# Kernel optimization log

Measured on AMD Instinct MI355X. Metric: run time of the kernel, lower is better.

Reference implementation:

```python
import jax, jax.numpy as jnp
import numpy as np

B, L, IDIM = 1, 1024, 2048
H, DK, DV, K = 16, 128, 128, 4
KEY_DIM = H * DK          # 2048
VAL_DIM = H * DV          # 2048
CONV_DIM = 2 * KEY_DIM + VAL_DIM  # 6144
EPS = 1e-6


def setup_inputs() -> dict:
    key = jax.random.key(0)
    ks = jax.random.split(key, 8)
    s = 0.02
    x = jax.random.normal(ks[0], (B, L, IDIM), jnp.float32)
    Wqkv = jax.random.normal(ks[1], (IDIM, CONV_DIM), jnp.float32) * s
    Wz = jax.random.normal(ks[2], (IDIM, VAL_DIM), jnp.float32) * s
    Wb = jax.random.normal(ks[3], (IDIM, H), jnp.float32) * s
    Wa = jax.random.normal(ks[4], (IDIM, H), jnp.float32) * s
    conv_w = jax.random.normal(ks[5], (CONV_DIM, 1, K), jnp.float32) * 0.2  # depthwise [O,I/g=1,K]
    A_log = jnp.log(jax.random.uniform(ks[6], (H,), jnp.float32, 0.1, 16.0))
    dt_bias = jnp.ones((H,), jnp.float32)
    norm_w = jnp.ones((DV,), jnp.float32)
    Wout = jax.random.normal(ks[7], (VAL_DIM, IDIM), jnp.float32) * s
    return dict(x=x, Wqkv=Wqkv, Wz=Wz, Wb=Wb, Wa=Wa, conv_w=conv_w,
                A_log=A_log, dt_bias=dt_bias, norm_w=norm_w, Wout=Wout)


def _l2norm(t):
    return t * jax.lax.rsqrt(jnp.sum(t * t, axis=-1, keepdims=True) + EPS)


def reference(x, Wqkv, Wz, Wb, Wa, conv_w, A_log, dt_bias, norm_w, Wout):
    b, l, _ = x.shape
    # fused QKV projection + causal depthwise conv + SiLU
    qkv = jnp.einsum('bld,dc->blc', x, Wqkv)                 # [B,L,CONV_DIM]
    qkv = jnp.transpose(qkv, (0, 2, 1))                      # [B,C,L]
    qkv = jax.lax.conv_general_dilated(
        qkv, conv_w, window_strides=(1,), padding=[(K - 1, 0)],
        dimension_numbers=('NCL', 'OIL', 'NCL'), feature_group_count=CONV_DIM)
    qkv = jax.nn.silu(jnp.transpose(qkv, (0, 2, 1)))         # [B,L,C]
    q, k, v = jnp.split(qkv, [KEY_DIM, 2 * KEY_DIM], axis=-1)

    z = jnp.einsum('bld,dv->blv', x, Wz)                     # [B,L,VAL_DIM]
    beta = jax.nn.sigmoid(jnp.einsum('bld,dh->blh', x, Wb))  # [B,L,H]
    A = -jnp.exp(A_log)                                      # [H]
    dt = jax.nn.softplus(jnp.einsum('bld,dh->blh', x, Wa) + dt_bias)
    g = dt * A                                               # [B,L,H] (negative)

    q = _l2norm(q.reshape(b, l, H, DK))
    k = _l2norm(k.reshape(b, l, H, DK))
    v = v.reshape(b, l, H, DV)
    scale = DK ** -0.5

    # time-major for scan: [L,B,H,...]
    qs = jnp.transpose(q, (1, 0, 2, 3)) * scale
    ks_ = jnp.transpose(k, (1, 0, 2, 3))
    vs = jnp.transpose(v, (1, 0, 2, 3))
    bs = jnp.transpose(beta, (1, 0, 2))
    gs = jnp.transpose(g, (1, 0, 2))

    M0 = jnp.zeros((b, H, DK, DV), jnp.float32)

    def step(M, inp):
        q_t, k_t, v_t, b_t, g_t = inp
        M = M * jnp.exp(g_t)[..., None, None]                    # decay
        Mk = jnp.einsum('bhd,bhdv->bhv', k_t, M)                 # readout of old mem
        M = M + jnp.einsum('bhd,bhv->bhdv', k_t, (v_t - Mk) * b_t[..., None])
        o_t = jnp.einsum('bhd,bhdv->bhv', q_t, M)
        return M, o_t

    _, out = jax.lax.scan(step, M0, (qs, ks_, vs, bs, gs))   # out: [L,B,H,DV]
    out = jnp.transpose(out, (1, 0, 2, 3))                   # [B,L,H,DV]

    # RMSNormGated: rms_norm(o) * weight * silu(z)
    zg = z.reshape(b, l, H, DV)
    rms = jax.lax.rsqrt(jnp.mean(out * out, axis=-1, keepdims=True) + EPS)
    out = (out * rms) * norm_w * jax.nn.silu(zg)

    out = out.reshape(b, l, VAL_DIM)
    return jnp.einsum('blv,vd->bld', out, Wout)
```

## Files before the change

kernel.cpp:

```cpp
#include <hip/hip_runtime.h>

typedef short bf16x8 __attribute__((ext_vector_type(8)));
typedef float f32x4 __attribute__((ext_vector_type(4)));
typedef float f32x2 __attribute__((ext_vector_type(2)));
typedef unsigned short u16;
typedef u16 u16x4 __attribute__((ext_vector_type(4)));

#define L_SEQ 1024
#define IDIM_ 2048
#define H_ 16
#define DK_ 128
#define DV_ 128
#define KEYD 2048
#define VALD 2048
#define CONVD 6144
#define QZD 8320
#define GCOL 8192
#define SCH 64
#define NSC (L_SEQ / SCH)

__device__ __forceinline__ u16 f2bf(float f) {
  union { float f; unsigned u; } v; v.f = f;
  unsigned r = v.u + 0x7FFF + ((v.u >> 16) & 1);
  return (u16)(r >> 16);
}

__device__ __forceinline__ float red16(float x) {
  union U { float f; int i; } a, t;
  a.f = x;
  t.i = __builtin_amdgcn_update_dpp(0, a.i, 0xB1, 0xF, 0xF, true); a.f += t.f;
  t.i = __builtin_amdgcn_update_dpp(0, a.i, 0x4E, 0xF, 0xF, true); a.f += t.f;
  t.i = __builtin_amdgcn_update_dpp(0, a.i, 0x141, 0xF, 0xF, true); a.f += t.f;
  t.i = __builtin_amdgcn_update_dpp(0, a.i, 0x140, 0xF, 0xF, true); a.f += t.f;
  return a.f;
}

__global__ __launch_bounds__(256) void prepcast_kernel(const float* __restrict__ x,
                                                       const float* __restrict__ Wqkv,
                                                       const float* __restrict__ Wz,
                                                       const float* __restrict__ Wb,
                                                       const float* __restrict__ Wa,
                                                       const float* __restrict__ Wout,
                                                       u16* __restrict__ xb,
                                                       u16* __restrict__ WcatT,
                                                       u16* __restrict__ WoutT) {
  __shared__ float tile[32][33];
  const int bid = blockIdx.x;
  if (bid < 2048) {
    int i = (bid * 256 + threadIdx.x) * 4;
    f32x4 v = *(const f32x4*)&x[i];
    u16x4 o = { f2bf(v[0]), f2bf(v[1]), f2bf(v[2]), f2bf(v[3]) };
    *(u16x4*)&xb[i] = o;
    return;
  }
  if (bid >= 22592) {
    size_t off = (size_t)8224 * IDIM_ + (size_t)(bid - 22592) * 8192 + threadIdx.x * 32;
    u16x4 z = {0, 0, 0, 0};
#pragma unroll
    for (int j = 0; j < 8; ++j) *(u16x4*)&WcatT[off + j * 4] = z;
    return;
  }
  if (bid >= 22528) {
    int by = bid - 22528;
    int r = threadIdx.x >> 3, c8 = threadIdx.x & 7;
    int row = by * 32 + r;
#pragma unroll
    for (int cc = 0; cc < 2; ++cc) {
      int c = cc * 8 + c8;
      WcatT[(size_t)(GCOL + c) * IDIM_ + row]      = f2bf(Wb[(size_t)row * 16 + c]);
      WcatT[(size_t)(GCOL + 16 + c) * IDIM_ + row] = f2bf(Wa[(size_t)row * 16 + c]);
    }
    return;
  }
  const float* W; u16* WT; int R, C, bx, by;
  if (bid < 14336) {
    int t = bid - 2048;  bx = t % 192; by = t / 192;
    W = Wqkv; WT = WcatT; R = IDIM_; C = CONVD;
  } else if (bid < 18432) {
    int t = bid - 14336; bx = t & 63; by = t >> 6;
    W = Wz; WT = WcatT + (size_t)CONVD * IDIM_; R = IDIM_; C = VALD;
  } else {
    int t = bid - 18432; bx = t & 63; by = t >> 6;
    W = Wout; WT = WoutT; R = VALD; C = IDIM_;
  }
  int c0 = bx * 32, r0 = by * 32;
  int tx = threadIdx.x & 31, ty = threadIdx.x >> 5;
#pragma unroll
  for (int j = 0; j < 4; ++j)
    tile[ty + j * 8][tx] = W[(size_t)(r0 + ty + j * 8) * C + c0 + tx];
  __syncthreads();
#pragma unroll
  for (int j = 0; j < 4; ++j)
    WT[(size_t)(c0 + ty + j * 8) * R + r0 + tx] = f2bf(tile[tx][ty + j * 8]);
}

__global__ __launch_bounds__(256) void gemm_bt_kernel(const u16* __restrict__ A,
                                                      const u16* __restrict__ B,
                                                      float* __restrict__ C,
                                                      int M, int N, int K) {
  __shared__ short As[128 * 72];
  __shared__ short Bs[128 * 72];
  const int tid = threadIdx.x;
  const int lane = tid & 63, wave = tid >> 6;
  const int wm = wave >> 1, wn = wave & 1;
  const int m0 = blockIdx.y * 128, n0 = blockIdx.x * 128;
  const int l15 = lane & 15, lhi = lane >> 4;

  f32x4 acc[4][4] = {};

  for (int k0 = 0; k0 < K; k0 += 64) {
    __syncthreads();
#pragma unroll
    for (int i = 0; i < 4; ++i) {
      int chunk = tid + i * 256;
      int row = chunk >> 3;
      int kc = (chunk & 7) * 8;
      *(bf16x8*)&As[row * 72 + kc] =
          *(const bf16x8*)&A[(size_t)(m0 + row) * K + k0 + kc];
      *(bf16x8*)&Bs[row * 72 + kc] =
          *(const bf16x8*)&B[(size_t)(n0 + row) * K + k0 + kc];
    }
    __syncthreads();
#pragma unroll
    for (int kk = 0; kk < 64; kk += 32) {
      const int koff = kk + lhi * 8;
      bf16x8 a[4], b[4];
#pragma unroll
      for (int m = 0; m < 4; ++m)
        a[m] = *(const bf16x8*)&As[(wm * 64 + m * 16 + l15) * 72 + koff];
#pragma unroll
      for (int n = 0; n < 4; ++n)
        b[n] = *(const bf16x8*)&Bs[(wn * 64 + n * 16 + l15) * 72 + koff];
#pragma unroll
      for (int m = 0; m < 4; ++m)
#pragma unroll
        for (int n = 0; n < 4; ++n)
          acc[m][n] = __builtin_amdgcn_mfma_f32_16x16x32_bf16(a[m], b[n], acc[m][n], 0, 0, 0);
    }
  }
#pragma unroll
  for (int m = 0; m < 4; ++m)
#pragma unroll
    for (int n = 0; n < 4; ++n)
#pragma unroll
      for (int j = 0; j < 4; ++j) {
        int row = m0 + wm * 64 + m * 16 + lhi * 4 + j;
        int col = n0 + wn * 64 + n * 16 + l15;
        C[(size_t)row * N + col] = acc[m][n][j];
      }
}

__global__ __launch_bounds__(256) void gemm_bt64_kernel(const u16* __restrict__ A,
                                                        const u16* __restrict__ B,
                                                        float* __restrict__ C,
                                                        int M, int N, int K, int cxl) {
  __shared__ short As[64 * 72];
  __shared__ short Bs[128 * 72];
  const int tid = threadIdx.x;
  const int lane = tid & 63, wave = tid >> 6;
  const int wm = wave >> 1, wn = wave & 1;
  const int bid = blockIdx.x;
  const int xcd = bid & 7, bi = bid >> 3;
  const int bx = (xcd << cxl) + (bi & ((1 << cxl) - 1));
  const int by = bi >> cxl;
  const int m0 = by * 64, n0 = bx * 128;
  const int l15 = lane & 15, lhi = lane >> 4;

  f32x4 acc[2][4] = {};

  for (int k0 = 0; k0 < K; k0 += 64) {
    __syncthreads();
#pragma unroll
    for (int i = 0; i < 2; ++i) {
      int chunk = tid + i * 256;
      int row = chunk >> 3;
      int kc = (chunk & 7) * 8;
      *(bf16x8*)&As[row * 72 + kc] =
          *(const bf16x8*)&A[(size_t)(m0 + row) * K + k0 + kc];
    }
#pragma unroll
    for (int i = 0; i < 4; ++i) {
      int chunk = tid + i * 256;
      int row = chunk >> 3;
      int kc = (chunk & 7) * 8;
      *(bf16x8*)&Bs[row * 72 + kc] =
          *(const bf16x8*)&B[(size_t)(n0 + row) * K + k0 + kc];
    }
    __syncthreads();
#pragma unroll
    for (int kk = 0; kk < 64; kk += 32) {
      const int koff = kk + lhi * 8;
      bf16x8 a[2], b[4];
#pragma unroll
      for (int m = 0; m < 2; ++m)
        a[m] = *(const bf16x8*)&As[(wm * 32 + m * 16 + l15) * 72 + koff];
#pragma unroll
      for (int n = 0; n < 4; ++n)
        b[n] = *(const bf16x8*)&Bs[(wn * 64 + n * 16 + l15) * 72 + koff];
#pragma unroll
      for (int m = 0; m < 2; ++m)
#pragma unroll
        for (int n = 0; n < 4; ++n)
          acc[m][n] = __builtin_amdgcn_mfma_f32_16x16x32_bf16(a[m], b[n], acc[m][n], 0, 0, 0);
    }
  }
#pragma unroll
  for (int m = 0; m < 2; ++m)
#pragma unroll
    for (int n = 0; n < 4; ++n)
#pragma unroll
      for (int j = 0; j < 4; ++j) {
        int row = m0 + wm * 32 + m * 16 + lhi * 4 + j;
        int col = n0 + wn * 64 + n * 16 + l15;
        C[(size_t)row * N + col] = acc[m][n][j];
      }
}

__global__ __launch_bounds__(256) void gatelite_kernel(const float* __restrict__ qkvz,
                                                       const float* __restrict__ A_log,
                                                       const float* __restrict__ dt_bias,
                                                       float* __restrict__ btT,
                                                       float* __restrict__ gT) {
  int gid = blockIdx.x * 256 + threadIdx.x;
  int l = gid >> 4, h = gid & 15;
  const float* row = qkvz + (size_t)l * QZD + GCOL;
  float b = row[h], a = row[16 + h];
  btT[h * L_SEQ + l] = 1.f / (1.f + expf(-b));
  float dtv = a + dt_bias[h];
  dtv = (dtv > 20.f) ? dtv : log1pf(expf(dtv));
  gT[h * L_SEQ + l] = -expf(A_log[h]) * dtv;
}

__global__ __launch_bounds__(256) void prep2_kernel(const float* __restrict__ qkvz,
                                                    const float* __restrict__ cw,
                                                    float* __restrict__ qn,
                                                    float* __restrict__ kn,
                                                    float* __restrict__ vT) {
  __shared__ float tile[32][33];
  const int bid = blockIdx.x;
  if (bid < 4096) {
    int wid = bid * 4 + (threadIdx.x >> 6);
    int lane = threadIdx.x & 63;
    int l = wid >> 4, h = wid & 15;
    const int cq = h * 128 + lane * 2;
    const int ck = KEYD + cq;
    const float* row0 = qkvz + (size_t)l * QZD;
    f32x4 wq0 = *(const f32x4*)&cw[cq * 4];
    f32x4 wq1 = *(const f32x4*)&cw[(cq + 1) * 4];
    f32x4 wk0 = *(const f32x4*)&cw[ck * 4];
    f32x4 wk1 = *(const f32x4*)&cw[(ck + 1) * 4];
    f32x2 xq = *(const f32x2*)&row0[cq];
    f32x2 xk = *(const f32x2*)&row0[ck];
    float q0 = xq[0] * wq0[3], q1 = xq[1] * wq1[3];
    float k0 = xk[0] * wk0[3], k1 = xk[1] * wk1[3];
    if (l >= 1) {
      f32x2 aq = *(const f32x2*)&row0[cq - QZD];
      f32x2 ak = *(const f32x2*)&row0[ck - QZD];
      q0 += aq[0] * wq0[2]; q1 += aq[1] * wq1[2];
      k0 += ak[0] * wk0[2]; k1 += ak[1] * wk1[2];
    }
    if (l >= 2) {
      f32x2 aq = *(const f32x2*)&row0[cq - 2 * QZD];
      f32x2 ak = *(const f32x2*)&row0[ck - 2 * QZD];
      q0 += aq[0] * wq0[1]; q1 += aq[1] * wq1[1];
      k0 += ak[0] * wk0[1]; k1 += ak[1] * wk1[1];
    }
    if (l >= 3) {
      f32x2 aq = *(const f32x2*)&row0[cq - 3 * QZD];
      f32x2 ak = *(const f32x2*)&row0[ck - 3 * QZD];
      q0 += aq[0] * wq0[0]; q1 += aq[1] * wq1[0];
      k0 += ak[0] * wk0[0]; k1 += ak[1] * wk1[0];
    }
    f32x2 qv = { q0 / (1.f + expf(-q0)), q1 / (1.f + expf(-q1)) };
    f32x2 kv = { k0 / (1.f + expf(-k0)), k1 / (1.f + expf(-k1)) };

    float ssq = qv[0] * qv[0] + qv[1] * qv[1];
    float ssk = kv[0] * kv[0] + kv[1] * kv[1];
#pragma unroll
    for (int s = 1; s < 64; s <<= 1) {
      ssq += __shfl_xor(ssq, s);
      ssk += __shfl_xor(ssk, s);
    }
    float scq = 0.08838834764831845f / sqrtf(ssq + 1e-6f);
    float sck = 1.f / sqrtf(ssk + 1e-6f);
    qv[0] *= scq; qv[1] *= scq;
    kv[0] *= sck; kv[1] *= sck;
    size_t base = ((size_t)h * L_SEQ + l) * 128 + lane * 2;
    *(f32x2*)&qn[base] = qv;
    *(f32x2*)&kn[base] = kv;
    return;
  }
  int t = bid - 4096;
  int c0 = (t & 63) * 32, l0 = (t >> 6) * 32;
  int tx = threadIdx.x & 31, ty = threadIdx.x >> 5;
  const int c = 2 * KEYD + c0 + tx;
  f32x4 w = *(const f32x4*)&cw[c * 4];
#pragma unroll
  for (int j = 0; j < 4; ++j) {
    int l = l0 + ty + j * 8;
    const float* p = qkvz + (size_t)l * QZD + c;
    float s = p[0] * w[3];
    if (l >= 1) s += p[-QZD] * w[2];
    if (l >= 2) s += p[-2 * QZD] * w[1];
    if (l >= 3) s += p[-3 * QZD] * w[0];
    tile[ty + j * 8][tx] = s / (1.f + expf(-s));
  }
  __syncthreads();
#pragma unroll
  for (int j = 0; j < 4; ++j)
    vT[(size_t)(c0 + ty + j * 8) * L_SEQ + l0 + tx] = tile[tx][ty + j * 8];
}

__global__ __launch_bounds__(256) void winv_kernel(const float* __restrict__ kn,
                                                   const float* __restrict__ gT,
                                                   const float* __restrict__ btT,
                                                   float* __restrict__ Wg) {
  __shared__ alignas(16) u16 kb[64][136];
  __shared__ float Nl[64][65];
  __shared__ float gsh[64], Gh[64], bts[64];

  const int tid = threadIdx.x;
  const int lane = tid & 63, wave = tid >> 6;
  const int l15 = lane & 15, lhi = lane >> 4;
  const int h = blockIdx.x & 15, sc = blockIdx.x >> 4;
  const int l0 = sc * SCH;

  {
    int t = tid >> 2, c0 = (tid & 3) * 32;
    const float* kr = kn + ((size_t)h * L_SEQ + l0 + t) * 128 + c0;
#pragma unroll
    for (int j = 0; j < 8; ++j) {
      f32x4 vk = *(const f32x4*)&kr[j * 4];
      u16x4 ok = { f2bf(vk[0]), f2bf(vk[1]), f2bf(vk[2]), f2bf(vk[3]) };
      *(u16x4*)&kb[t][c0 + j * 4] = ok;
    }
  }
  if (tid < 64) {
    gsh[tid] = gT[h * L_SEQ + l0 + tid];
    bts[tid] = btT[h * L_SEQ + l0 + tid];
  }
  __syncthreads();
  if (tid < 64) {
    float a = 0.f;
    for (int u = 0; u <= tid; ++u) a += gsh[u];
    Gh[tid] = a;
  }
  __syncthreads();

  f32x4 acc1[2][2] = {};
  const int wm = wave >> 1, wn = wave & 1;
#pragma unroll
  for (int kk = 0; kk < 128; kk += 32) {
    const int koff = kk + lhi * 8;
    bf16x8 a[2], b[2];
#pragma unroll
    for (int m = 0; m < 2; ++m)
      a[m] = *(const bf16x8*)&kb[wm * 32 + m * 16 + l15][koff];
#pragma unroll
    for (int n = 0; n < 2; ++n)
      b[n] = *(const bf16x8*)&kb[wn * 32 + n * 16 + l15][koff];
#pragma unroll
    for (int m = 0; m < 2; ++m)
#pragma unroll
      for (int n = 0; n < 2; ++n)
        acc1[m][n] = __builtin_amdgcn_mfma_f32_16x16x32_bf16(a[m], b[n], acc1[m][n], 0, 0, 0);
  }
#pragma unroll
  for (int m = 0; m < 2; ++m)
#pragma unroll
    for (int n = 0; n < 2; ++n)
#pragma unroll
      for (int j = 0; j < 4; ++j) {
        int t = wm * 32 + m * 16 + lhi * 4 + j;
        int s = wn * 32 + n * 16 + l15;
        Nl[t][s] = (s < t) ? bts[t] * expf(Gh[t] - Gh[s]) * acc1[m][n][j] : 0.f;
      }
  __syncthreads();

  if (wave == 0) {
    float w[64];
    w[0] = (lane == 0) ? 1.f : 0.f;
#pragma unroll
    for (int t = 1; t < 64; ++t) {
      float a0 = (lane == t) ? 1.f : 0.f, a1 = 0.f;
#pragma unroll
      for (int s = 0; s + 1 < t; s += 2) {
        a0 = fmaf(-Nl[t][s], w[s], a0);
        a1 = fmaf(-Nl[t][s + 1], w[s + 1], a1);
      }
      if (t & 1) a0 = fmaf(-Nl[t][t - 1], w[t - 1], a0);
      w[t] = a0 + a1;
    }
    size_t base = (size_t)(sc * 16 + h) * 4096 + (size_t)lane * 64;
#pragma unroll
    for (int s = 0; s < 64; ++s) Wg[base + s] = w[s];
  }
}

__global__ __launch_bounds__(256) void wyscan_kernel(const float* __restrict__ kn,
                                                     const float* __restrict__ vT,
                                                     const float* __restrict__ gT,
                                                     const float* __restrict__ btT,
                                                     const float* __restrict__ Wg,
                                                     float* __restrict__ Mb,
                                                     float* __restrict__ DbT) {
  __shared__ float klds[128][65];
  __shared__ float Mlds[128][9];
  __shared__ float WldsT[64][65];
  __shared__ float rlds[64][9];
  __shared__ float dlds[64][9];
  __shared__ float gsh[64], Gh[64], bts[64];

  const int tid = threadIdx.x;
  const int lane = tid & 63, wave = tid >> 6;
  const int h = blockIdx.x & 15, dvb = blockIdx.x >> 4;
  const int dv0 = dvb * 8;
  const int dva = wave * 2, dvb2 = wave * 2 + 1;

  for (int i = tid; i < 128 * 9; i += 256) Mlds[i / 9][i % 9] = 0.f;
  __syncthreads();

#pragma unroll 1
  for (int c = 0; c < NSC; ++c) {
    const int l0 = c * SCH;
    {
      int t = tid >> 2, c0 = (tid & 3) * 32;
      const float* kr = kn + ((size_t)h * L_SEQ + l0 + t) * 128 + c0;
#pragma unroll
      for (int j = 0; j < 32; ++j) klds[c0 + j][t] = kr[j];
    }
    {
      size_t base = (size_t)(c * 16 + h) * 4096;
      for (int i = tid; i < 4096; i += 256) WldsT[i >> 6][i & 63] = Wg[base + i];
    }
    if (tid < 64) {
      gsh[tid] = gT[h * L_SEQ + l0 + tid];
      bts[tid] = btT[h * L_SEQ + l0 + tid];
    }
    {
      int dv = tid >> 5, dk0 = (tid & 31) * 4;
      float* mr = Mb + (((size_t)(c * 16 + h)) * 128 + dv0 + dv) * 128 + dk0;
#pragma unroll
      for (int j = 0; j < 4; ++j) mr[j] = Mlds[dk0 + j][dv];
    }
    __syncthreads();
    if (tid == 0) {
      float a = 0.f;
      for (int u = 0; u < 64; ++u) { a += gsh[u]; Gh[u] = a; }
    }
    __syncthreads();

    {
      const int t = lane;
      float a0 = 0.f, a1 = 0.f;
      for (int dk = 0; dk < 128; ++dk) {
        float kv = klds[dk][t];
        a0 = fmaf(kv, Mlds[dk][dva], a0);
        a1 = fmaf(kv, Mlds[dk][dvb2], a1);
      }
      float egt = expf(Gh[t]);
      float bt = bts[t];
      float v0 = vT[(size_t)(h * 128 + dv0 + dva) * L_SEQ + l0 + t];
      float v1 = vT[(size_t)(h * 128 + dv0 + dvb2) * L_SEQ + l0 + t];
      rlds[t][dva]  = bt * (v0 - egt * a0);
      rlds[t][dvb2] = bt * (v1 - egt * a1);
    }
    __syncthreads();

    {
      const int t = lane;
      float a0 = 0.f, a1 = 0.f;
      for (int s = 0; s < 64; ++s) {
        float wv = WldsT[s][t];
        a0 = fmaf(wv, rlds[s][dva], a0);
        a1 = fmaf(wv, rlds[s][dvb2], a1);
      }
      DbT[(size_t)(h * 128 + dv0 + dva) * L_SEQ + l0 + t]  = a0;
      DbT[(size_t)(h * 128 + dv0 + dvb2) * L_SEQ + l0 + t] = a1;
      float e63t = expf(Gh[63] - Gh[t]);
      dlds[t][dva]  = a0 * e63t;
      dlds[t][dvb2] = a1 * e63t;
    }
    __syncthreads();

    {
      const float E63 = expf(Gh[63]);
#pragma unroll
      for (int rep = 0; rep < 2; ++rep) {
        const int dk = lane + rep * 64;
#pragma unroll
        for (int dvi = 0; dvi < 2; ++dvi) {
          const int dv = wave * 2 + dvi;
          float acc = E63 * Mlds[dk][dv];
          for (int s = 0; s < 64; ++s)
            acc = fmaf(klds[dk][s], dlds[s][dv], acc);
          Mlds[dk][dv] = acc;
        }
      }
    }
    __syncthreads();
  }
}

__global__ __launch_bounds__(256) void opass_kernel(const float* __restrict__ qn,
                                                    const float* __restrict__ kn,
                                                    const float* __restrict__ DbT,
                                                    const float* __restrict__ gT,
                                                    const float* __restrict__ Mb,
                                                    const float* __restrict__ qkvz,
                                                    const float* __restrict__ norm_w,
                                                    u16* __restrict__ gn) {
  __shared__ alignas(16) u16 qsb[64][136];
  __shared__ alignas(16) u16 bbuf[128][136];
  __shared__ alignas(16) u16 Asb[64][72];
  __shared__ float gsh[64], Gh[64];
  __shared__ float ssr[2][64];

  const int tid = threadIdx.x;
  const int lane = tid & 63, wave = tid >> 6;
  const int l15 = lane & 15, lhi = lane >> 4;
  const int h = blockIdx.x & 15, sc = blockIdx.x >> 4;
  const int l0 = sc * SCH;

  {
    int t = tid >> 2, c0 = (tid & 3) * 32;
    const float* qr = qn + ((size_t)h * L_SEQ + l0 + t) * 128 + c0;
    const float* kr = kn + ((size_t)h * L_SEQ + l0 + t) * 128 + c0;
#pragma unroll
    for (int j = 0; j < 8; ++j) {
      f32x4 vq = *(const f32x4*)&qr[j * 4];
      f32x4 vk = *(const f32x4*)&kr[j * 4];
      u16x4 oq = { f2bf(vq[0]), f2bf(vq[1]), f2bf(vq[2]), f2bf(vq[3]) };
      u16x4 ok = { f2bf(vk[0]), f2bf(vk[1]), f2bf(vk[2]), f2bf(vk[3]) };
      *(u16x4*)&qsb[t][c0 + j * 4] = oq;
      *(u16x4*)&bbuf[t][c0 + j * 4] = ok;
    }
  }
  if (tid < 64) gsh[tid] = gT[h * L_SEQ + l0 + tid];
  __syncthreads();
  if (tid < 64) {
    float a = 0.f;
    for (int u = 0; u <= tid; ++u) a += gsh[u];
    Gh[tid] = a;
  }
  __syncthreads();

  f32x4 acc1[2][2] = {};
  const int wm = wave >> 1, wn = wave & 1;
#pragma unroll
  for (int kk = 0; kk < 128; kk += 32) {
    const int koff = kk + lhi * 8;
    bf16x8 a[2], b[2];
#pragma unroll
    for (int m = 0; m < 2; ++m)
      a[m] = *(const bf16x8*)&qsb[wm * 32 + m * 16 + l15][koff];
#pragma unroll
    for (int n = 0; n < 2; ++n)
      b[n] = *(const bf16x8*)&bbuf[wn * 32 + n * 16 + l15][koff];
#pragma unroll
    for (int m = 0; m < 2; ++m)
#pragma unroll
      for (int n = 0; n < 2; ++n)
        acc1[m][n] = __builtin_amdgcn_mfma_f32_16x16x32_bf16(a[m], b[n], acc1[m][n], 0, 0, 0);
  }
#pragma unroll
  for (int m = 0; m < 2; ++m)
#pragma unroll
    for (int n = 0; n < 2; ++n)
#pragma unroll
      for (int j = 0; j < 4; ++j) {
        int t = wm * 32 + m * 16 + lhi * 4 + j;
        int s = wn * 32 + n * 16 + l15;
        float a = (s <= t) ? acc1[m][n][j] * expf(Gh[t] - Gh[s]) : 0.f;
        Asb[t][s] = f2bf(a);
      }
  __syncthreads();

  {
    int dv = tid >> 1, c0 = (tid & 1) * 64;
    const float* mr = Mb + (((size_t)sc * 16 + h) * 128 + dv) * 128 + c0;
#pragma unroll
    for (int j = 0; j < 16; ++j) {
      f32x4 v = *(const f32x4*)&mr[j * 4];
      u16x4 o = { f2bf(v[0]), f2bf(v[1]), f2bf(v[2]), f2bf(v[3]) };
      *(u16x4*)&bbuf[dv][c0 + j * 4] = o;
    }
  }
  __syncthreads();

  f32x4 acc[2][4] = {};
#pragma unroll
  for (int kk = 0; kk < 128; kk += 32) {
    const int koff = kk + lhi * 8;
    bf16x8 a[2], b[4];
#pragma unroll
    for (int m = 0; m < 2; ++m)
      a[m] = *(const bf16x8*)&qsb[wm * 32 + m * 16 + l15][koff];
#pragma unroll
    for (int n = 0; n < 4; ++n)
      b[n] = *(const bf16x8*)&bbuf[wn * 64 + n * 16 + l15][koff];
#pragma unroll
    for (int m = 0; m < 2; ++m)
#pragma unroll
      for (int n = 0; n < 4; ++n)
        acc[m][n] = __builtin_amdgcn_mfma_f32_16x16x32_bf16(a[m], b[n], acc[m][n], 0, 0, 0);
  }
#pragma unroll
  for (int m = 0; m < 2; ++m) {
#pragma unroll
    for (int j = 0; j < 4; ++j) {
      int t = wm * 32 + m * 16 + lhi * 4 + j;
      float sc1 = expf(Gh[t]);
#pragma unroll
      for (int n = 0; n < 4; ++n) acc[m][n][j] *= sc1;
    }
  }
  __syncthreads();

  {
    int dv = tid >> 1, c0 = (tid & 1) * 32;
    const float* dr = DbT + (size_t)(h * 128 + dv) * L_SEQ + l0 + c0;
#pragma unroll
    for (int j = 0; j < 8; ++j) {
      f32x4 v = *(const f32x4*)&dr[j * 4];
      u16x4 o = { f2bf(v[0]), f2bf(v[1]), f2bf(v[2]), f2bf(v[3]) };
      *(u16x4*)&bbuf[dv][c0 + j * 4] = o;
    }
  }
  __syncthreads();

#pragma unroll
  for (int kk = 0; kk < 64; kk += 32) {
    const int koff = kk + lhi * 8;
    bf16x8 a[2], b[4];
#pragma unroll
    for (int m = 0; m < 2; ++m)
      a[m] = *(const bf16x8*)&Asb[wm * 32 + m * 16 + l15][koff];
#pragma unroll
    for (int n = 0; n < 4; ++n)
      b[n] = *(const bf16x8*)&bbuf[wn * 64 + n * 16 + l15][koff];
#pragma unroll
    for (int m = 0; m < 2; ++m)
#pragma unroll
      for (int n = 0; n < 4; ++n)
        acc[m][n] = __builtin_amdgcn_mfma_f32_16x16x32_bf16(a[m], b[n], acc[m][n], 0, 0, 0);
  }

  float pr[2][4];
#pragma unroll
  for (int m = 0; m < 2; ++m)
#pragma unroll
    for (int j = 0; j < 4; ++j) {
      float p = 0.f;
#pragma unroll
      for (int n = 0; n < 4; ++n) p = fmaf(acc[m][n][j], acc[m][n][j], p);
      pr[m][j] = red16(p);
    }
  if (l15 == 0) {
#pragma unroll
    for (int m = 0; m < 2; ++m)
#pragma unroll
      for (int j = 0; j < 4; ++j)
        ssr[wn][wm * 32 + m * 16 + lhi * 4 + j] = pr[m][j];
  }
  __syncthreads();
#pragma unroll
  for (int m = 0; m < 2; ++m)
#pragma unroll
    for (int j = 0; j < 4; ++j) {
      int t = wm * 32 + m * 16 + lhi * 4 + j;
      float ss = ssr[0][t] + ssr[1][t];
      float r = 1.f / sqrtf(ss * (1.f / 128.f) + 1e-6f);
      const float* zp = qkvz + (size_t)(l0 + t) * QZD + CONVD + h * 128;
      u16* dst = gn + (size_t)(l0 + t) * VALD + h * 128;
#pragma unroll
      for (int n = 0; n < 4; ++n) {
        int dv = wn * 64 + n * 16 + l15;
        float z = zp[dv];
        float sil = z / (1.f + expf(-z));
        dst[dv] = f2bf(acc[m][n][j] * r * norm_w[dv] * sil);
      }
    }
}

extern "C" void kernel_launch(void* const* d_in, const int* in_sizes, int n_in,
                              void* d_out, int out_size, void* d_ws, size_t ws_size,
                              hipStream_t stream) {
  const float* x      = (const float*)d_in[0];
  const float* Wqkv   = (const float*)d_in[1];
  const float* Wz     = (const float*)d_in[2];
  const float* Wb     = (const float*)d_in[3];
  const float* Wa     = (const float*)d_in[4];
  const float* conv_w = (const float*)d_in[5];
  const float* A_log  = (const float*)d_in[6];
  const float* dt_bias= (const float*)d_in[7];
  const float* norm_w = (const float*)d_in[8];
  const float* Wout   = (const float*)d_in[9];
  float* out = (float*)d_out;

  char* ws = (char*)d_ws;
  size_t off = 0;
  auto alloc = [&](size_t bytes) {
    void* p = ws + off;
    off = (off + bytes + 255) & ~(size_t)255;
    return p;
  };
  u16* xb     = (u16*)alloc((size_t)L_SEQ * IDIM_ * 2);
  u16* WcatT  = (u16*)alloc((size_t)QZD * IDIM_ * 2);
  u16* WoutT  = (u16*)alloc((size_t)IDIM_ * VALD * 2);
  float* qkvz = (float*)alloc((size_t)L_SEQ * QZD * 4);
  float* qn   = (float*)alloc((size_t)H_ * L_SEQ * 128 * 4);
  float* kn   = (float*)alloc((size_t)H_ * L_SEQ * 128 * 4);
  float* vT   = (float*)alloc((size_t)H_ * 128 * L_SEQ * 4);
  float* btT  = (float*)alloc((size_t)L_SEQ * H_ * 4);
  float* gTb  = (float*)alloc((size_t)L_SEQ * H_ * 4);
  float* Wgb  = (float*)alloc((size_t)NSC * H_ * 64 * 64 * 4);
  float* Mb   = (float*)alloc((size_t)NSC * H_ * 128 * 128 * 4);
  float* DbT  = (float*)alloc((size_t)H_ * 128 * L_SEQ * 4);
  u16* gn     = (u16*)alloc((size_t)L_SEQ * VALD * 2);

  prepcast_kernel<<<22616, 256, 0, stream>>>(x, Wqkv, Wz, Wb, Wa, Wout, xb, WcatT, WoutT);

  gemm_bt_kernel<<<dim3(QZD / 128, L_SEQ / 128), 256, 0, stream>>>(xb, WcatT, qkvz, L_SEQ, QZD, IDIM_);

  gatelite_kernel<<<64, 256, 0, stream>>>(qkvz, A_log, dt_bias, btT, gTb);

  prep2_kernel<<<6144, 256, 0, stream>>>(qkvz, conv_w, qn, kn, vT);

  winv_kernel<<<NSC * H_, 256, 0, stream>>>(kn, gTb, btT, Wgb);
  wyscan_kernel<<<256, 256, 0, stream>>>(kn, vT, gTb, btT, Wgb, Mb, DbT);

  opass_kernel<<<NSC * H_, 256, 0, stream>>>(qn, kn, DbT, gTb, Mb, qkvz, norm_w, gn);

  gemm_bt64_kernel<<<256, 256, 0, stream>>>(gn, WoutT, out, L_SEQ, IDIM_, VALD, 1);
}
```

Measured before the change: 363.2 us.

## Rewrite chunked WY scan with bf16 MFMA and one block per head

The inter-chunk state scan moves from scalar FP32 LDS dot products spread across 256 blocks (16 heads x 16 dv slices) to bf16 MFMA matrix products, with one block per head holding the full 128x128 state in registers. Each chunk runs three small GEMMs (k·M, W·r, kᵀ·d) on matrix cores, and the state is kept as an FP32 copy plus a bf16 copy in LDS. The aim is to cut the FP32 ALU and LDS cost of the sequential scan. In exchange, the grid shrinks to 16 blocks, leaving most CUs idle, and the recurrent state loses precision from bf16 operands.

```diff
diff --git a/kernel.cpp b/kernel.cpp
--- a/kernel.cpp
+++ b/kernel.cpp
@@ -404,99 +404,174 @@
                                                      const float* __restrict__ Wg,
                                                      float* __restrict__ Mb,
                                                      float* __restrict__ DbT) {
-  __shared__ float klds[128][65];
-  __shared__ float Mlds[128][9];
-  __shared__ float WldsT[64][65];
-  __shared__ float rlds[64][9];
-  __shared__ float dlds[64][9];
+  __shared__ alignas(16) u16 kb[64][136];
+  __shared__ alignas(16) u16 kbT[128][72];
+  __shared__ alignas(16) u16 Wbf[64][72];
+  __shared__ alignas(16) u16 rTb[128][72];
+  __shared__ alignas(16) u16 ddT[128][72];
+  __shared__ alignas(16) u16 MbfT[128][136];
   __shared__ float gsh[64], Gh[64], bts[64];
 
   const int tid = threadIdx.x;
   const int lane = tid & 63, wave = tid >> 6;
-  const int h = blockIdx.x & 15, dvb = blockIdx.x >> 4;
-  const int dv0 = dvb * 8;
-  const int dva = wave * 2, dvb2 = wave * 2 + 1;
-
-  for (int i = tid; i < 128 * 9; i += 256) Mlds[i / 9][i % 9] = 0.f;
+  const int l15 = lane & 15, lhi = lane >> 4;
+  const int wm = wave >> 1, wn = wave & 1;
+  const int h = blockIdx.x;
+
+  for (int i = tid; i < 128 * 136; i += 256) (&MbfT[0][0])[i] = 0;
+  f32x4 Mreg[4][4];
+#pragma unroll
+  for (int m = 0; m < 4; ++m)
+#pragma unroll
+    for (int n = 0; n < 4; ++n) Mreg[m][n] = (f32x4){0.f, 0.f, 0.f, 0.f};
   __syncthreads();
 
 #pragma unroll 1
   for (int c = 0; c < NSC; ++c) {
     const int l0 = c * SCH;
+#pragma unroll
+    for (int m = 0; m < 4; ++m)
+#pragma unroll
+      for (int n = 0; n < 4; ++n) {
+        int dv = wn * 64 + n * 16 + l15;
+        int dk0 = wm * 64 + m * 16 + lhi * 4;
+        *(f32x4*)&Mb[(((size_t)(c * 16 + h)) * 128 + dv) * 128 + dk0] = Mreg[m][n];
+      }
     {
       int t = tid >> 2, c0 = (tid & 3) * 32;
       const float* kr = kn + ((size_t)h * L_SEQ + l0 + t) * 128 + c0;
 #pragma unroll
-      for (int j = 0; j < 32; ++j) klds[c0 + j][t] = kr[j];
+      for (int j = 0; j < 32; ++j) {
+        u16 kv = f2bf(kr[j]);
+        kb[t][c0 + j] = kv;
+        kbT[c0 + j][t] = kv;
+      }
     }
     {
+      int t = tid >> 2, s0 = (tid & 3) * 16;
       size_t base = (size_t)(c * 16 + h) * 4096;
-      for (int i = tid; i < 4096; i += 256) WldsT[i >> 6][i & 63] = Wg[base + i];
+#pragma unroll
+      for (int i = 0; i < 16; ++i)
+        Wbf[t][s0 + i] = f2bf(Wg[base + (size_t)(s0 + i) * 64 + t]);
     }
     if (tid < 64) {
       gsh[tid] = gT[h * L_SEQ + l0 + tid];
       bts[tid] = btT[h * L_SEQ + l0 + tid];
     }
+    __syncthreads();
+    if (tid < 64) {
+      float a = 0.f;
+      for (int u = 0; u <= tid; ++u) a += gsh[u];
+      Gh[tid] = a;
+    }
+    __syncthreads();
+
     {
-      int dv = tid >> 5, dk0 = (tid & 31) * 4;
-      float* mr = Mb + (((size_t)(c * 16 + h)) * 128 + dv0 + dv) * 128 + dk0;
-#pragma unroll
-      for (int j = 0; j < 4; ++j) mr[j] = Mlds[dk0 + j][dv];
+      f32x4 acc[2][4] = {};
+#pragma unroll
+      for (int kk = 0; kk < 128; kk += 32) {
+        const int koff = kk + lhi * 8;
+        bf16x8 a[2], b[4];
+#pragma unroll
+        for (int m = 0; m < 2; ++m)
+          a[m] = *(const bf16x8*)&kb[wm * 32 + m * 16 + l15][koff];
+#pragma unroll
+        for (int n = 0; n < 4; ++n)
+          b[n] = *(const bf16x8*)&MbfT[wn * 64 + n * 16 + l15][koff];
+#pragma unroll
+        for (int m = 0; m < 2; ++m)
+#pragma unroll
+          for (int n = 0; n < 4; ++n)
+            acc[m][n] = __builtin_amdgcn_mfma_f32_16x16x32_bf16(a[m], b[n], acc[m][n], 0, 0, 0);
+      }
+#pragma unroll
+      for (int m = 0; m < 2; ++m)
+#pragma unroll
+        for (int n = 0; n < 4; ++n) {
+          int dv = wn * 64 + n * 16 + l15;
+          int t0 = wm * 32 + m * 16 + lhi * 4;
+          f32x4 v4 = *(const f32x4*)&vT[(size_t)(h * 128 + dv) * L_SEQ + l0 + t0];
+#pragma unroll
+          for (int j = 0; j < 4; ++j) {
+            int t = t0 + j;
+            float r = bts[t] * (v4[j] - expf(Gh[t]) * acc[m][n][j]);
+            rTb[dv][t] = f2bf(r);
+          }
+        }
     }
     __syncthreads();
-    if (tid == 0) {
-      float a = 0.f;
-      for (int u = 0; u < 64; ++u) { a += gsh[u]; Gh[u] = a; }
-    }
-    __syncthreads();
 
     {
-      const int t = lane;
-      float a0 = 0.f, a1 = 0.f;
-      for (int dk = 0; dk < 128; ++dk) {
-        float kv = klds[dk][t];
-        a0 = fmaf(kv, Mlds[dk][dva], a0);
-        a1 = fmaf(kv, Mlds[dk][dvb2], a1);
-      }
-      float egt = expf(Gh[t]);
-      float bt = bts[t];
-      float v0 = vT[(size_t)(h * 128 + dv0 + dva) * L_SEQ + l0 + t];
-      float v1 = vT[(size_t)(h * 128 + dv0 + dvb2) * L_SEQ + l0 + t];
-      rlds[t][dva]  = bt * (v0 - egt * a0);
-      rlds[t][dvb2] = bt * (v1 - egt * a1);
-    }
-    __syncthreads();
-
-    {
-      const int t = lane;
-      float a0 = 0.f, a1 = 0.f;
-      for (int s = 0; s < 64; ++s) {
-        float wv = WldsT[s][t];
-        a0 = fmaf(wv, rlds[s][dva], a0);
-        a1 = fmaf(wv, rlds[s][dvb2], a1);
-      }
-      DbT[(size_t)(h * 128 + dv0 + dva) * L_SEQ + l0 + t]  = a0;
-      DbT[(size_t)(h * 128 + dv0 + dvb2) * L_SEQ + l0 + t] = a1;
-      float e63t = expf(Gh[63] - Gh[t]);
-      dlds[t][dva]  = a0 * e63t;
-      dlds[t][dvb2] = a1 * e63t;
+      f32x4 acc[2][4] = {};
+#pragma unroll
+      for (int kk = 0; kk < 64; kk += 32) {
+        const int koff = kk + lhi * 8;
+        bf16x8 a[2], b[4];
+#pragma unroll
+        for (int m = 0; m < 2; ++m)
+          a[m] = *(const bf16x8*)&Wbf[wm * 32 + m * 16 + l15][koff];
+#pragma unroll
+        for (int n = 0; n < 4; ++n)
+          b[n] = *(const bf16x8*)&rTb[wn * 64 + n * 16 + l15][koff];
+#pragma unroll
+        for (int m = 0; m < 2; ++m)
+#pragma unroll
+          for (int n = 0; n < 4; ++n)
+            acc[m][n] = __builtin_amdgcn_mfma_f32_16x16x32_bf16(a[m], b[n], acc[m][n], 0, 0, 0);
+      }
+      const float G63 = Gh[63];
+#pragma unroll
+      for (int m = 0; m < 2; ++m)
+#pragma unroll
+        for (int n = 0; n < 4; ++n) {
+          int dv = wn * 64 + n * 16 + l15;
+          int t0 = wm * 32 + m * 16 + lhi * 4;
+          *(f32x4*)&DbT[(size_t)(h * 128 + dv) * L_SEQ + l0 + t0] = acc[m][n];
+#pragma unroll
+          for (int j = 0; j < 4; ++j) {
+            int t = t0 + j;
+            ddT[dv][t] = f2bf(acc[m][n][j] * expf(G63 - Gh[t]));
+          }
+        }
     }
     __syncthreads();
 
     {
       const float E63 = expf(Gh[63]);
-#pragma unroll
-      for (int rep = 0; rep < 2; ++rep) {
-        const int dk = lane + rep * 64;
-#pragma unroll
-        for (int dvi = 0; dvi < 2; ++dvi) {
-          const int dv = wave * 2 + dvi;
-          float acc = E63 * Mlds[dk][dv];
-          for (int s = 0; s < 64; ++s)
-            acc = fmaf(klds[dk][s], dlds[s][dv], acc);
-          Mlds[dk][dv] = acc;
+      f32x4 acc[4][4];
+#pragma unroll
+      for (int m = 0; m < 4; ++m)
+#pragma unroll
+        for (int n = 0; n < 4; ++n)
+#pragma unroll
+          for (int j = 0; j < 4; ++j) acc[m][n][j] = E63 * Mreg[m][n][j];
+#pragma unroll
+      for (int kk = 0; kk < 64; kk += 32) {
+        const int koff = kk + lhi * 8;
+        bf16x8 a[4], b[4];
+#pragma unroll
+        for (int m = 0; m < 4; ++m)
+          a[m] = *(const bf16x8*)&kbT[wm * 64 + m * 16 + l15][koff];
+#pragma unroll
+        for (int n = 0; n < 4; ++n)
+          b[n] = *(const bf16x8*)&ddT[wn * 64 + n * 16 + l15][koff];
+#pragma unroll
+        for (int m = 0; m < 4; ++m)
+#pragma unroll
+          for (int n = 0; n < 4; ++n)
+            acc[m][n] = __builtin_amdgcn_mfma_f32_16x16x32_bf16(a[m], b[n], acc[m][n], 0, 0, 0);
+      }
+#pragma unroll
+      for (int m = 0; m < 4; ++m)
+#pragma unroll
+        for (int n = 0; n < 4; ++n) {
+          Mreg[m][n] = acc[m][n];
+          int dv = wn * 64 + n * 16 + l15;
+          int dk0 = wm * 64 + m * 16 + lhi * 4;
+#pragma unroll
+          for (int j = 0; j < 4; ++j)
+            MbfT[dv][dk0 + j] = f2bf(acc[m][n][j]);
         }
-      }
     }
     __syncthreads();
   }
@@ -728,7 +803,7 @@
   prep2_kernel<<<6144, 256, 0, stream>>>(qkvz, conv_w, qn, kn, vT);
 
   winv_kernel<<<NSC * H_, 256, 0, stream>>>(kn, gTb, btT, Wgb);
-  wyscan_kernel<<<256, 256, 0, stream>>>(kn, vT, gTb, btT, Wgb, Mb, DbT);
+  wyscan_kernel<<<H_, 256, 0, stream>>>(kn, vT, gTb, btT, Wgb, Mb, DbT);
 
   opass_kernel<<<NSC * H_, 256, 0, stream>>>(qn, kn, DbT, gTb, Mb, qkvz, norm_w, gn);
 
```

Result: no change. 362.8 us (-0.1%).
